# Kernel tuning notes

Measured on AMD Instinct MI355X. Metric: run time of the kernel, lower is better.

The kernel has to match this reference:

```python
import jax, jax.numpy as jnp
import numpy as np
import math

N_HEAD = 16
N_EMBD = 1024
N_LATENTS = 64
HEAD_DIM = N_EMBD // N_HEAD  # 64
ROPE_THETA = 10000.0


def setup_inputs() -> dict:
    key = jax.random.key(0)
    ks = jax.random.split(key, 6)
    B, T = 4, 4096
    x = jax.random.normal(ks[0], (B, T, N_EMBD), dtype=jnp.float32)
    # torch Linear weights applied as x @ W with W: [in, out] (equivalent up to init)
    s = 1.0 / math.sqrt(N_EMBD)
    Wk = jax.random.normal(ks[1], (N_EMBD, N_EMBD), dtype=jnp.float32) * s
    Wv = jax.random.normal(ks[2], (N_EMBD, N_EMBD), dtype=jnp.float32) * s
    Wg = jax.random.normal(ks[3], (N_EMBD, N_HEAD * N_LATENTS), dtype=jnp.float32) * s
    Wp = jax.random.normal(ks[4], (N_EMBD, N_EMBD), dtype=jnp.float32) * s
    latent_q = jax.random.normal(ks[5], (1, N_LATENTS, N_HEAD, HEAD_DIM), dtype=jnp.float32)
    return {"x": x, "latent_q": latent_q, "Wk": Wk, "Wv": Wv, "Wg": Wg, "Wp": Wp}


def _rope_interleaved(k, theta):
    # k: [B, T, H, D]; interleaved pairs rotated by position-dependent angles
    B, T, H, D = k.shape
    inv_freq = 1.0 / (theta ** (jnp.arange(0, D, 2, dtype=jnp.float32) / D))  # [D/2]
    ang = jnp.arange(T, dtype=jnp.float32)[:, None] * inv_freq[None, :]       # [T, D/2]
    cos = jnp.cos(ang)[None, :, None, :]
    sin = jnp.sin(ang)[None, :, None, :]
    k2 = k.reshape(B, T, H, D // 2, 2)
    kr = jnp.stack([k2[..., 0] * cos - k2[..., 1] * sin,
                    k2[..., 0] * sin + k2[..., 1] * cos], axis=-1)
    return kr.reshape(B, T, H, D).astype(k.dtype)


def reference(x, latent_q, Wk, Wv, Wg, Wp):
    B, T, C = x.shape
    H, D, L = N_HEAD, HEAD_DIM, N_LATENTS
    k = (x @ Wk).reshape(B, T, H, D)
    v = (x @ Wv).reshape(B, T, H, D)
    gates = jax.nn.softmax((x @ Wg).reshape(B, T, H, L), axis=-1)  # [B,T,H,L]
    k = _rope_interleaved(k, ROPE_THETA)
    q = jnp.broadcast_to(latent_q, (B, L, H, D)).transpose(0, 2, 1, 3)  # [B,H,L,D]
    kt = k.transpose(0, 2, 1, 3)  # [B,H,T,D]
    vt = v.transpose(0, 2, 1, 3)  # [B,H,T,D]
    scale = 1.0 / jnp.sqrt(jnp.asarray(D, dtype=x.dtype))
    scores = jnp.einsum('bhld,bhtd->bhlt', q, kt) * scale  # [B,H,L,T]
    # PyTorch SDPA is_causal with L_q != L_kv: top-left aligned tril(ones(L, T))
    causal = jnp.arange(T)[None, :] <= jnp.arange(L)[:, None]  # [L,T]
    scores = jnp.where(causal[None, None], scores, -jnp.inf)
    attn = jax.nn.softmax(scores, axis=-1)
    attn_out = jnp.einsum('bhlt,bhtd->bhld', attn, vt)  # [B,H,L,D]
    gates_t = gates.transpose(0, 2, 1, 3)  # [B,H,T,L]
    weighted = jnp.einsum('bhld,bhtl->bhtd', attn_out, gates_t)  # [B,H,T,D]
    out = weighted.transpose(0, 2, 1, 3).reshape(B, T, C)
    return out @ Wp
```

## Files before the change

### kernel.cpp

```cpp
#include <hip/hip_runtime.h>
#include <hip/hip_bf16.h>


typedef __attribute__((ext_vector_type(8))) short bf16x8;
typedef __attribute__((ext_vector_type(4))) float f32x4;
typedef __attribute__((ext_vector_type(4))) unsigned short us4;

__device__ __forceinline__ void gll16(const void* g, void* l) {
  __builtin_amdgcn_global_load_lds((const __attribute__((address_space(1))) void*)g,
                                   (__attribute__((address_space(3))) void*)l, 16, 0, 0);
}

__global__ __launch_bounds__(256)
void prep_kernel(const float* __restrict__ x, __hip_bfloat16* __restrict__ xb,
                 const float* __restrict__ Wg, const float* __restrict__ Wk,
                 const float* __restrict__ Wv,
                 __hip_bfloat16* __restrict__ WgT, __hip_bfloat16* __restrict__ WkT,
                 __hip_bfloat16* __restrict__ WvT) {
  const int bid = blockIdx.x, tid = threadIdx.x;
  if (bid < 2048) {
    const int stride = 2048 * 256;
    for (int i = bid * 256 + tid; i < 4194304; i += stride) {
      float4 f = reinterpret_cast<const float4*>(x)[i];
      union { __hip_bfloat16 h[4]; us4 v; } u;
      u.h[0] = __float2bfloat16(f.x);
      u.h[1] = __float2bfloat16(f.y);
      u.h[2] = __float2bfloat16(f.z);
      u.h[3] = __float2bfloat16(f.w);
      reinterpret_cast<us4*>(xb)[i] = u.v;
    }
  } else {
    const int t = bid - 2048;
    const int z = t >> 10, rem = t & 1023;
    const float* W = (z == 0) ? Wg : ((z == 1) ? Wk : Wv);
    __hip_bfloat16* Wt = (z == 0) ? WgT : ((z == 1) ? WkT : WvT);
    __shared__ float tile[32][33];
    const int bx = (rem & 31) * 32, by = (rem >> 5) * 32;
    const int tx = tid & 31, ty = tid >> 5;
    #pragma unroll
    for (int j = 0; j < 32; j += 8)
      tile[ty + j][tx] = W[(size_t)(by + ty + j) * 1024 + bx + tx];
    __syncthreads();
    #pragma unroll
    for (int j = 0; j < 32; j += 8)
      Wt[(size_t)(bx + ty + j) * 1024 + by + tx] = __float2bfloat16(tile[tx][ty + j]);
  }
}

template <int EPI>
__global__ __launch_bounds__(512, 2)
void gemm256(const __hip_bfloat16* __restrict__ A, const __hip_bfloat16* __restrict__ Bt,
             void* __restrict__ Cv, int K, int ldc,
             long long astride, long long bstride, long long cstride) {
  __shared__ __align__(16) unsigned short SA[2][256 * 64];
  __shared__ __align__(16) unsigned short SB[2][256 * 64];
  const int tid = threadIdx.x;
  const int lane = tid & 63;
  const int w = tid >> 6;
  const int wm = w >> 2, wn = w & 3;
  const int lr = lane & 15, lk = lane >> 4;
  const int m0 = blockIdx.x * 256, n0 = blockIdx.y * 256;
  const long long b = blockIdx.z;
  const __hip_bfloat16* Ab = A + b * astride;
  const __hip_bfloat16* Bb = Bt + b * bstride;

  f32x4 acc[8][4] = {};

  const int NT = K >> 6;
  int buf = 0;

  auto STAGE = [&](int bsel, int kt) {
    #pragma unroll
    for (int r = 0; r < 4; ++r) {
      int c = r * 512 + tid;
      int row = c >> 3, slot = c & 7;
      int gch = slot ^ (row & 7);
      gll16(Ab + (size_t)(m0 + row) * K + kt + gch * 8, (char*)&SA[bsel][0] + c * 16);
      gll16(Bb + (size_t)(n0 + row) * K + kt + gch * 8, (char*)&SB[bsel][0] + c * 16);
    }
  };

  STAGE(0, 0);
  __syncthreads();

  for (int t = 0; t < NT; ++t) {
    if (t + 1 < NT) STAGE(buf ^ 1, (t + 1) << 6);

    bf16x8 bfr[2][4];
    #pragma unroll
    for (int kk = 0; kk < 2; ++kk)
      #pragma unroll
      for (int ni = 0; ni < 4; ++ni) {
        int row = wn * 64 + ni * 16 + lr;
        int ch = (kk * 4 + lk) ^ (row & 7);
        bfr[kk][ni] = *(const bf16x8*)&SB[buf][row * 64 + ch * 8];
      }
    #pragma unroll
    for (int mi = 0; mi < 8; ++mi) {
      int row = wm * 128 + mi * 16 + lr;
      int ch0 = lk ^ (row & 7);
      int ch1 = (4 + lk) ^ (row & 7);
      bf16x8 a0 = *(const bf16x8*)&SA[buf][row * 64 + ch0 * 8];
      bf16x8 a1 = *(const bf16x8*)&SA[buf][row * 64 + ch1 * 8];
      #pragma unroll
      for (int ni = 0; ni < 4; ++ni)
        acc[mi][ni] = __builtin_amdgcn_mfma_f32_16x16x32_bf16(a0, bfr[0][ni], acc[mi][ni], 0, 0, 0);
      #pragma unroll
      for (int ni = 0; ni < 4; ++ni)
        acc[mi][ni] = __builtin_amdgcn_mfma_f32_16x16x32_bf16(a1, bfr[1][ni], acc[mi][ni], 0, 0, 0);
    }
    __syncthreads();
    buf ^= 1;
  }

  if (EPI == 0) {
    float* C = (float*)Cv + b * cstride;
    #pragma unroll
    for (int mi = 0; mi < 8; ++mi) {
      int r = m0 + wm * 128 + mi * 16 + lk * 4;
      #pragma unroll
      for (int ni = 0; ni < 4; ++ni) {
        int c = n0 + wn * 64 + ni * 16 + lr;
        #pragma unroll
        for (int jj = 0; jj < 4; ++jj)
          C[(size_t)(r + jj) * ldc + c] = acc[mi][ni][jj];
      }
    }
  } else {
    __hip_bfloat16* C = (__hip_bfloat16*)Cv + b * cstride;
    #pragma unroll
    for (int mi = 0; mi < 8; ++mi) {
      #pragma unroll
      for (int jj = 0; jj < 4; ++jj) {
        float mx = -3.0e38f;
        #pragma unroll
        for (int ni = 0; ni < 4; ++ni) mx = fmaxf(mx, acc[mi][ni][jj]);
        mx = fmaxf(mx, __shfl_xor(mx, 1));
        mx = fmaxf(mx, __shfl_xor(mx, 2));
        mx = fmaxf(mx, __shfl_xor(mx, 4));
        mx = fmaxf(mx, __shfl_xor(mx, 8));
        float e[4];
        float s = 0.f;
        #pragma unroll
        for (int ni = 0; ni < 4; ++ni) { e[ni] = __expf(acc[mi][ni][jj] - mx); s += e[ni]; }
        s += __shfl_xor(s, 1);
        s += __shfl_xor(s, 2);
        s += __shfl_xor(s, 4);
        s += __shfl_xor(s, 8);
        float inv = 1.0f / s;
        int r = m0 + wm * 128 + mi * 16 + lk * 4 + jj;
        #pragma unroll
        for (int ni = 0; ni < 4; ++ni)
          C[(size_t)r * ldc + n0 + wn * 64 + ni * 16 + lr] = __float2bfloat16(e[ni] * inv);
      }
    }
  }
}

__global__ __launch_bounds__(256)
void gemm_kv(const __hip_bfloat16* __restrict__ A, const __hip_bfloat16* __restrict__ Bt,
             float* __restrict__ kvp) {
  __shared__ __align__(16) unsigned short As[128 * 32];
  __shared__ __align__(16) unsigned short Bs[128 * 32];
  const int tid = threadIdx.x;
  const int lane = tid & 63;
  const int w = tid >> 6;
  const int wm = w >> 1, wn = w & 1;
  const int lr = lane & 15, lk = lane >> 4;
  const int m0 = blockIdx.x * 128, n0 = blockIdx.y * 128;
  const int ks = blockIdx.z;
  const int K = 1024;

  f32x4 acc[4][4] = {};
  const int r0 = tid >> 2;
  const int c8 = (tid & 3) * 8;

  auto xrow = [&](int rg) { return (size_t)(rg >> 6) * 4096 + (rg & 63); };

  for (int ki = 0; ki < 4; ++ki) {
    int kt = ks * 128 + ki * 32;
    __syncthreads();
    gll16(A + xrow(m0 + r0) * K + kt + c8,      (char*)As + (w * 64) * 16);
    gll16(Bt + (size_t)(n0 + r0) * K + kt + c8, (char*)Bs + (w * 64) * 16);
    gll16(A + xrow(m0 + 64 + r0) * K + kt + c8,      (char*)As + (256 + w * 64) * 16);
    gll16(Bt + (size_t)(n0 + 64 + r0) * K + kt + c8, (char*)Bs + (256 + w * 64) * 16);
    __syncthreads();

    bf16x8 af[4], bf[4];
    #pragma unroll
    for (int mi = 0; mi < 4; ++mi)
      af[mi] = *(const bf16x8*)&As[(wm * 64 + mi * 16 + lr) * 32 + lk * 8];
    #pragma unroll
    for (int ni = 0; ni < 4; ++ni)
      bf[ni] = *(const bf16x8*)&Bs[(wn * 64 + ni * 16 + lr) * 32 + lk * 8];
    #pragma unroll
    for (int mi = 0; mi < 4; ++mi)
      #pragma unroll
      for (int ni = 0; ni < 4; ++ni)
        acc[mi][ni] = __builtin_amdgcn_mfma_f32_16x16x32_bf16(af[mi], bf[ni], acc[mi][ni], 0, 0, 0);
  }

  float* C = kvp + (size_t)ks * 256 * 2048;
  #pragma unroll
  for (int mi = 0; mi < 4; ++mi) {
    int r = m0 + wm * 64 + mi * 16 + lk * 4;
    #pragma unroll
    for (int ni = 0; ni < 4; ++ni) {
      int c = n0 + wn * 64 + ni * 16 + lr;
      #pragma unroll
      for (int jj = 0; jj < 4; ++jj)
        C[(size_t)(r + jj) * 2048 + c] = acc[mi][ni][jj];
    }
  }
}

__global__ __launch_bounds__(256)
void attn_mt(const float* __restrict__ kvp, const float* __restrict__ lq,
             const float* __restrict__ Wp, __hip_bfloat16* __restrict__ Mt) {
  const int ct = blockIdx.x, h = blockIdx.y, b = blockIdx.z;
  __shared__ float Ks[64][64];
  __shared__ float Vs[64][64];
  __shared__ float S[64][65];
  __shared__ float Pt[64][65];
  const int tid = threadIdx.x;

  {
    int r = tid >> 4;
    int c4 = (tid & 15) * 4;
    int i0 = c4 >> 1;
    float inv0 = exp2f(-13.287712379549449f * ((float)i0 * (1.0f / 32.0f)));
    float inv1 = exp2f(-13.287712379549449f * ((float)(i0 + 1) * (1.0f / 32.0f)));
    #pragma unroll
    for (int j = 0; j < 4; ++j) {
      int row = j * 16 + r;
      float4 kf = make_float4(0.f, 0.f, 0.f, 0.f);
      float4 vf = make_float4(0.f, 0.f, 0.f, 0.f);
      #pragma unroll
      for (int ks = 0; ks < 8; ++ks) {
        const float* base = kvp + ((size_t)ks * 256 + b * 64 + row) * 2048 + h * 64;
        float4 kp = *(const float4*)(base + c4);
        float4 vp = *(const float4*)(base + 1024 + c4);
        kf.x += kp.x; kf.y += kp.y; kf.z += kp.z; kf.w += kp.w;
        vf.x += vp.x; vf.y += vp.y; vf.z += vp.z; vf.w += vp.w;
      }
      float a0 = (float)row * inv0, a1 = (float)row * inv1;
      float s0 = sinf(a0), c0 = cosf(a0), s1 = sinf(a1), c1 = cosf(a1);
      *(float4*)&Ks[row][c4] = make_float4(kf.x * c0 - kf.y * s0, kf.x * s0 + kf.y * c0,
                                           kf.z * c1 - kf.w * s1, kf.z * s1 + kf.w * c1);
      *(float4*)&Vs[row][c4] = vf;
    }
  }
  __syncthreads();

  {
    const int w = tid >> 6, l = tid & 63;
    float q[64];
    const float4* lq4 = (const float4*)(lq + ((size_t)l * 16 + h) * 64);
    #pragma unroll
    for (int i = 0; i < 16; ++i) {
      float4 f = lq4[i];
      q[4 * i] = f.x; q[4 * i + 1] = f.y; q[4 * i + 2] = f.z; q[4 * i + 3] = f.w;
    }
    #pragma unroll
    for (int tl = 0; tl < 16; ++tl) {
      int t = w * 16 + tl;
      float a = 0.f;
      #pragma unroll
      for (int d4 = 0; d4 < 16; ++d4) {
        float4 kf = *(const float4*)&Ks[t][d4 * 4];
        a += q[4 * d4] * kf.x + q[4 * d4 + 1] * kf.y + q[4 * d4 + 2] * kf.z + q[4 * d4 + 3] * kf.w;
      }
      S[l][t] = a * 0.125f;
    }
  }
  __syncthreads();

  {
    const int l = tid >> 2, c = tid & 3;
    float sv[16];
    float mx = -3.0e38f;
    #pragma unroll
    for (int i = 0; i < 16; ++i) {
      int t = c * 16 + i;
      sv[i] = S[l][t];
      if (t <= l) mx = fmaxf(mx, sv[i]);
    }
    mx = fmaxf(mx, __shfl_xor(mx, 1));
    mx = fmaxf(mx, __shfl_xor(mx, 2));
    float sum = 0.f;
    float e[16];
    #pragma unroll
    for (int i = 0; i < 16; ++i) {
      int t = c * 16 + i;
      e[i] = (t <= l) ? __expf(sv[i] - mx) : 0.f;
      sum += e[i];
    }
    sum += __shfl_xor(sum, 1);
    sum += __shfl_xor(sum, 2);
    float inv = 1.0f / sum;
    #pragma unroll
    for (int i = 0; i < 16; ++i) Pt[c * 16 + i][l] = e[i] * inv;
  }
  __syncthreads();

  {
    const int w = tid >> 6, l = tid & 63;
    float o[16];
    #pragma unroll
    for (int i = 0; i < 16; ++i) o[i] = 0.f;
    for (int t = 0; t < 64; ++t) {
      float p = Pt[t][l];
      #pragma unroll
      for (int d4 = 0; d4 < 4; ++d4) {
        float4 vf = *(const float4*)&Vs[t][w * 16 + d4 * 4];
        o[4 * d4]     += p * vf.x;
        o[4 * d4 + 1] += p * vf.y;
        o[4 * d4 + 2] += p * vf.z;
        o[4 * d4 + 3] += p * vf.w;
      }
    }
    #pragma unroll
    for (int i = 0; i < 16; ++i) S[l][w * 16 + i] = o[i];
  }
  __syncthreads();

  {
    const int c = ct * 256 + tid;
    for (int lc = 0; lc < 4; ++lc) {
      float a2[16];
      #pragma unroll
      for (int li = 0; li < 16; ++li) a2[li] = 0.f;
      for (int d = 0; d < 64; ++d) {
        float wv = Wp[(size_t)(h * 64 + d) * 1024 + c];
        #pragma unroll
        for (int li = 0; li < 16; ++li) a2[li] += S[lc * 16 + li][d] * wv;
      }
      size_t base = ((size_t)b * 1024 + c) * 1024 + h * 64 + lc * 16;
      #pragma unroll
      for (int li = 0; li < 16; ++li) Mt[base + li] = __float2bfloat16(a2[li]);
    }
  }
}

extern "C" void kernel_launch(void* const* d_in, const int* in_sizes, int n_in,
                              void* d_out, int out_size, void* d_ws, size_t ws_size,
                              hipStream_t stream) {
  const float* x  = (const float*)d_in[0];
  const float* lq = (const float*)d_in[1];
  const float* Wk = (const float*)d_in[2];
  const float* Wv = (const float*)d_in[3];
  const float* Wg = (const float*)d_in[4];
  const float* Wp = (const float*)d_in[5];
  float* out = (float*)d_out;

  char* w = (char*)d_ws;
  __hip_bfloat16* xb   = (__hip_bfloat16*)(w);
  __hip_bfloat16* G    = (__hip_bfloat16*)(w + 33554432);
  __hip_bfloat16* WgT  = (__hip_bfloat16*)(w + 67108864);
  __hip_bfloat16* WkvT = (__hip_bfloat16*)(w + 69206016);
  __hip_bfloat16* Mt   = (__hip_bfloat16*)(w + 73400320);
  float* kvp = out;

  prep_kernel<<<5120, 256, 0, stream>>>(x, xb, Wg, Wk, Wv, WgT, WkvT, WkvT + 1024 * 1024);

  gemm256<1><<<dim3(64, 4, 1), 512, 0, stream>>>(xb, WgT, G, 1024, 1024, 0LL, 0LL, 0LL);

  gemm_kv<<<dim3(2, 16, 8), 256, 0, stream>>>(xb, WkvT, kvp);

  attn_mt<<<dim3(4, 16, 4), 256, 0, stream>>>(kvp, lq, Wp, Mt);

  gemm256<0><<<dim3(16, 4, 4), 512, 0, stream>>>(G, Mt, out, 1024, 1024,
                                                 4096LL * 1024, 1024LL * 1024, 4096LL * 1024);
}
```

Before: 159.7 us.

## Split attention from Mt construction and build Mt with bf16 MFMA

The attention kernel now runs once per (head, batch) instead of being recomputed for each of the four column tiles, and writes its output to a bf16 buffer. A new MFMA kernel multiplies that output by a pre-transposed bf16 Wp (transposed in prep_kernel) to form Mt, replacing the scalar FP32 loop. The goal is to remove redundant attention work and the slow scalar projection. The cost is an extra kernel launch, a larger prep kernel, and bf16 rounding of the attention output before projection.

```diff
diff --git a/kernel.cpp b/kernel.cpp
--- a/kernel.cpp
+++ b/kernel.cpp
@@ -5,6 +5,7 @@
 typedef __attribute__((ext_vector_type(8))) short bf16x8;
 typedef __attribute__((ext_vector_type(4))) float f32x4;
 typedef __attribute__((ext_vector_type(4))) unsigned short us4;
+typedef __attribute__((ext_vector_type(8))) unsigned short us8;
 
 __device__ __forceinline__ void gll16(const void* g, void* l) {
   __builtin_amdgcn_global_load_lds((const __attribute__((address_space(1))) void*)g,
@@ -14,9 +15,9 @@
 __global__ __launch_bounds__(256)
 void prep_kernel(const float* __restrict__ x, __hip_bfloat16* __restrict__ xb,
                  const float* __restrict__ Wg, const float* __restrict__ Wk,
-                 const float* __restrict__ Wv,
+                 const float* __restrict__ Wv, const float* __restrict__ Wp,
                  __hip_bfloat16* __restrict__ WgT, __hip_bfloat16* __restrict__ WkT,
-                 __hip_bfloat16* __restrict__ WvT) {
+                 __hip_bfloat16* __restrict__ WvT, __hip_bfloat16* __restrict__ WpT) {
   const int bid = blockIdx.x, tid = threadIdx.x;
   if (bid < 2048) {
     const int stride = 2048 * 256;
@@ -32,8 +33,8 @@
   } else {
     const int t = bid - 2048;
     const int z = t >> 10, rem = t & 1023;
-    const float* W = (z == 0) ? Wg : ((z == 1) ? Wk : Wv);
-    __hip_bfloat16* Wt = (z == 0) ? WgT : ((z == 1) ? WkT : WvT);
+    const float* W = (z == 0) ? Wg : ((z == 1) ? Wk : ((z == 2) ? Wv : Wp));
+    __hip_bfloat16* Wt = (z == 0) ? WgT : ((z == 1) ? WkT : ((z == 2) ? WvT : WpT));
     __shared__ float tile[32][33];
     const int bx = (rem & 31) * 32, by = (rem >> 5) * 32;
     const int tx = tid & 31, ty = tid >> 5;
@@ -215,9 +216,9 @@
 }
 
 __global__ __launch_bounds__(256)
-void attn_mt(const float* __restrict__ kvp, const float* __restrict__ lq,
-             const float* __restrict__ Wp, __hip_bfloat16* __restrict__ Mt) {
-  const int ct = blockIdx.x, h = blockIdx.y, b = blockIdx.z;
+void attn_kernel(const float* __restrict__ kvp, const float* __restrict__ lq,
+                 __hip_bfloat16* __restrict__ aoB) {
+  const int h = blockIdx.x, b = blockIdx.y;
   __shared__ float Ks[64][64];
   __shared__ float Vs[64][64];
   __shared__ float S[64][65];
@@ -319,25 +320,77 @@
         o[4 * d4 + 3] += p * vf.w;
       }
     }
-    #pragma unroll
-    for (int i = 0; i < 16; ++i) S[l][w * 16 + i] = o[i];
+    union { __hip_bfloat16 h[16]; us8 v[2]; } u;
+    #pragma unroll
+    for (int i = 0; i < 16; ++i) u.h[i] = __float2bfloat16(o[i]);
+    us8* dst = (us8*)(aoB + (((size_t)b * 16 + h) * 64 + l) * 64 + w * 16);
+    dst[0] = u.v[0];
+    dst[1] = u.v[1];
+  }
+}
+
+__global__ __launch_bounds__(256)
+void build_mt_mfma(const __hip_bfloat16* __restrict__ aoB, const __hip_bfloat16* __restrict__ WpT,
+                   __hip_bfloat16* __restrict__ Mt) {
+  __shared__ __align__(16) unsigned short SW[256 * 64];
+  __shared__ __align__(16) unsigned short SAo[64 * 64];
+  const int ct = blockIdx.x, h = blockIdx.y, b = blockIdx.z;
+  const int tid = threadIdx.x;
+  const int lane = tid & 63;
+  const int w = tid >> 6;
+  const int lr = lane & 15, lk = lane >> 4;
+
+  #pragma unroll
+  for (int j = 0; j < 8; ++j) {
+    int c2 = j * 256 + tid;
+    int row = c2 >> 3, slot = c2 & 7;
+    int gch = slot ^ (row & 7);
+    gll16(WpT + (size_t)(ct * 256 + row) * 1024 + h * 64 + gch * 8, (char*)SW + c2 * 16);
+  }
+  const __hip_bfloat16* aob = aoB + (((size_t)b * 16 + h) * 64) * 64;
+  #pragma unroll
+  for (int j = 0; j < 2; ++j) {
+    int c2 = j * 256 + tid;
+    int row = c2 >> 3, slot = c2 & 7;
+    int gch = slot ^ (row & 7);
+    gll16(aob + (size_t)row * 64 + gch * 8, (char*)SAo + c2 * 16);
   }
   __syncthreads();
 
-  {
-    const int c = ct * 256 + tid;
-    for (int lc = 0; lc < 4; ++lc) {
-      float a2[16];
-      #pragma unroll
-      for (int li = 0; li < 16; ++li) a2[li] = 0.f;
-      for (int d = 0; d < 64; ++d) {
-        float wv = Wp[(size_t)(h * 64 + d) * 1024 + c];
-        #pragma unroll
-        for (int li = 0; li < 16; ++li) a2[li] += S[lc * 16 + li][d] * wv;
-      }
-      size_t base = ((size_t)b * 1024 + c) * 1024 + h * 64 + lc * 16;
-      #pragma unroll
-      for (int li = 0; li < 16; ++li) Mt[base + li] = __float2bfloat16(a2[li]);
+  f32x4 acc[4][4] = {};
+  bf16x8 bfr[2][4];
+  #pragma unroll
+  for (int kk = 0; kk < 2; ++kk)
+    #pragma unroll
+    for (int ni = 0; ni < 4; ++ni) {
+      int row = ni * 16 + lr;
+      int ch = (kk * 4 + lk) ^ (row & 7);
+      bfr[kk][ni] = *(const bf16x8*)&SAo[row * 64 + ch * 8];
+    }
+  #pragma unroll
+  for (int mi = 0; mi < 4; ++mi) {
+    int row = w * 64 + mi * 16 + lr;
+    int ch0 = lk ^ (row & 7);
+    int ch1 = (4 + lk) ^ (row & 7);
+    bf16x8 a0 = *(const bf16x8*)&SW[row * 64 + ch0 * 8];
+    bf16x8 a1 = *(const bf16x8*)&SW[row * 64 + ch1 * 8];
+    #pragma unroll
+    for (int ni = 0; ni < 4; ++ni)
+      acc[mi][ni] = __builtin_amdgcn_mfma_f32_16x16x32_bf16(a0, bfr[0][ni], acc[mi][ni], 0, 0, 0);
+    #pragma unroll
+    for (int ni = 0; ni < 4; ++ni)
+      acc[mi][ni] = __builtin_amdgcn_mfma_f32_16x16x32_bf16(a1, bfr[1][ni], acc[mi][ni], 0, 0, 0);
+  }
+
+  #pragma unroll
+  for (int mi = 0; mi < 4; ++mi) {
+    int c = ct * 256 + w * 64 + mi * 16 + lk * 4;
+    #pragma unroll
+    for (int ni = 0; ni < 4; ++ni) {
+      int l = ni * 16 + lr;
+      #pragma unroll
+      for (int jj = 0; jj < 4; ++jj)
+        Mt[((size_t)b * 1024 + c + jj) * 1024 + h * 64 + l] = __float2bfloat16(acc[mi][ni][jj]);
     }
   }
 }
@@ -358,16 +411,21 @@
   __hip_bfloat16* G    = (__hip_bfloat16*)(w + 33554432);
   __hip_bfloat16* WgT  = (__hip_bfloat16*)(w + 67108864);
   __hip_bfloat16* WkvT = (__hip_bfloat16*)(w + 69206016);
-  __hip_bfloat16* Mt   = (__hip_bfloat16*)(w + 73400320);
+  __hip_bfloat16* WpT  = (__hip_bfloat16*)(w + 73400320);
+  __hip_bfloat16* Mt   = (__hip_bfloat16*)(w + 75497472);
+  __hip_bfloat16* aoB  = (__hip_bfloat16*)(w + 83886080);
   float* kvp = out;
 
-  prep_kernel<<<5120, 256, 0, stream>>>(x, xb, Wg, Wk, Wv, WgT, WkvT, WkvT + 1024 * 1024);
+  prep_kernel<<<6144, 256, 0, stream>>>(x, xb, Wg, Wk, Wv, Wp,
+                                        WgT, WkvT, WkvT + 1024 * 1024, WpT);
 
   gemm256<1><<<dim3(64, 4, 1), 512, 0, stream>>>(xb, WgT, G, 1024, 1024, 0LL, 0LL, 0LL);
 
   gemm_kv<<<dim3(2, 16, 8), 256, 0, stream>>>(xb, WkvT, kvp);
 
-  attn_mt<<<dim3(4, 16, 4), 256, 0, stream>>>(kvp, lq, Wp, Mt);
+  attn_kernel<<<dim3(16, 4), 256, 0, stream>>>(kvp, lq, aoB);
+
+  build_mt_mfma<<<dim3(4, 16, 4), 256, 0, stream>>>(aoB, WpT, Mt);
 
   gemm256<0><<<dim3(16, 4, 4), 512, 0, stream>>>(G, Mt, out, 1024, 1024,
                                                  4096LL * 1024, 1024LL * 1024, 4096LL * 1024);
```

Measured after the change: 132.3 us. -17.1%, faster.
